# Optimization experiments

Hardware: AMD Instinct MI355X
Metric: run time of the kernel (lower is better)

Reference implementation:

```python
import jax, jax.numpy as jnp
import numpy as np

N = 170000          # n_users + n_entities
NNZ = 2720000       # edges in sparse A_in (avg degree 16)
DIMS = [64, 64, 32, 16]
NEG_SLOPE = 0.01    # nn.LeakyReLU default
EPS = 1e-12         # F.normalize eps


def setup_inputs() -> dict:
    key = jax.random.key(0)
    ks = jax.random.split(key, 20)
    inp = {
        "embeddings": jax.random.normal(ks[0], (N, DIMS[0]), jnp.float32) * 0.1,
        "a_vals": jax.random.uniform(ks[1], (NNZ,), jnp.float32) / 16.0,  # ~row-normalized
    }
    # bi-interaction layer params, stored (in, out) so y = x @ W + b
    i = 2
    for l in range(3):
        din, dout = DIMS[l], DIMS[l + 1]
        s = 1.0 / np.sqrt(din)
        inp[f"w1_{l}"] = jax.random.normal(ks[i], (din, dout), jnp.float32) * s; i += 1
        inp[f"b1_{l}"] = jnp.zeros((dout,), jnp.float32)
        inp[f"w2_{l}"] = jax.random.normal(ks[i], (din, dout), jnp.float32) * s; i += 1
        inp[f"b2_{l}"] = jnp.zeros((dout,), jnp.float32)
    inp["a_rows"] = jax.random.randint(ks[i], (NNZ,), 0, N, jnp.int32); i += 1
    inp["a_cols"] = jax.random.randint(ks[i], (NNZ,), 0, N, jnp.int32)
    return inp


def _leaky(x):
    return jnp.where(x >= 0, x, NEG_SLOPE * x)


def _l2norm(x):
    n = jnp.sqrt(jnp.sum(x * x, axis=1, keepdims=True))
    return x / jnp.maximum(n, EPS)


def _spmm(vals, rows, cols, emb):
    # sparse A (COO) @ emb : gather source rows, scale, scatter-add to dest rows
    msgs = vals[:, None] * emb[cols]          # (nnz, d)
    return jax.ops.segment_sum(msgs, rows, num_segments=N)


def reference(embeddings, a_vals,
              w1_0, b1_0, w2_0, b2_0,
              w1_1, b1_1, w2_1, b2_1,
              w1_2, b1_2, w2_2, b2_2,
              a_rows, a_cols):
    layers = [(w1_0, b1_0, w2_0, b2_0),
              (w1_1, b1_1, w2_1, b2_1),
              (w1_2, b1_2, w2_2, b2_2)]
    ego = embeddings
    all_embed = [ego]
    for (w1, b1, w2, b2) in layers:
        side = _spmm(a_vals, a_rows, a_cols, ego)            # (N, d_in)
        sum_e = _leaky((ego + side) @ w1 + b1)               # bi-interaction
        bi_e = _leaky((ego * side) @ w2 + b2)
        ego = sum_e + bi_e                                   # dropout = identity (eval)
        all_embed.append(_l2norm(ego))
    return jnp.concatenate(all_embed, axis=1)                # (N, 176)
```

## Files before the change

### kernel.cpp

```cpp
#include <hip/hip_runtime.h>
#include <hip/hip_bf16.h>

#define NEG_SLOPE 0.01f
#define L2EPS 1e-12f
#define SCAN_CHUNK 2048
#define PART_CH 8192
#define BSHIFT 9

__device__ __forceinline__ unsigned short f2bf(float f) {
    unsigned u = __float_as_uint(f);
    return (unsigned short)((u + 0x7fffu + ((u >> 16) & 1u)) >> 16);
}


__global__ void scan_sum(const int* __restrict__ counts, int* __restrict__ partials, int n) {
    __shared__ int red[256];
    int base = blockIdx.x * SCAN_CHUNK;
    int s = 0;
    for (int i = threadIdx.x; i < SCAN_CHUNK; i += 256) {
        int idx = base + i;
        s += (idx < n) ? counts[idx] : 0;
    }
    red[threadIdx.x] = s; __syncthreads();
    for (int o = 128; o > 0; o >>= 1) {
        if (threadIdx.x < o) red[threadIdx.x] += red[threadIdx.x + o];
        __syncthreads();
    }
    if (threadIdx.x == 0) partials[blockIdx.x] = red[0];
}

__global__ void scan_partials(int* __restrict__ partials, int nb, int* __restrict__ out, int n) {
    if (threadIdx.x == 0 && blockIdx.x == 0) {
        int run = 0;
        for (int i = 0; i < nb; i++) { int v = partials[i]; partials[i] = run; run += v; }
        out[n] = run;
    }
}

__global__ void scan_apply(const int* __restrict__ counts, const int* __restrict__ partials,
                           int* __restrict__ out, int n) {
    __shared__ int lsum[256];
    int base = blockIdx.x * SCAN_CHUNK;
    int t = threadIdx.x;
    int my[8];
    int s = 0;
    int tb = base + t * 8;
    for (int i = 0; i < 8; i++) { int idx = tb + i; int v = (idx < n) ? counts[idx] : 0; my[i] = v; s += v; }
    lsum[t] = s; __syncthreads();
    for (int o = 1; o < 256; o <<= 1) {
        int v = (t >= o) ? lsum[t - o] : 0;
        __syncthreads();
        lsum[t] += v;
        __syncthreads();
    }
    int excl = lsum[t] - s + partials[blockIdx.x];
    for (int i = 0; i < 8; i++) {
        int idx = tb + i;
        if (idx < n) { out[idx] = excl; excl += my[i]; }
    }
}


__global__ void part_hist(const int* __restrict__ rows, int* __restrict__ hist,
                          int nnz, int nchunks, int B) {
    __shared__ int h[512];
    int c = blockIdx.x;
    for (int i = threadIdx.x; i < B; i += 256) h[i] = 0;
    __syncthreads();
    int s = c * PART_CH, e = min(s + PART_CH, nnz);
    for (int i = s + threadIdx.x; i < e; i += 256) atomicAdd(&h[rows[i] >> BSHIFT], 1);
    __syncthreads();
    for (int b = threadIdx.x; b < B; b += 256) hist[b * nchunks + c] = h[b];
}

__global__ void part_scatter(const int* __restrict__ rows, const int* __restrict__ cols,
                             const float* __restrict__ vals, const int* __restrict__ hscan,
                             int2* __restrict__ tmp, int nnz, int nchunks, int B) {
    __shared__ int cur[512];
    int c = blockIdx.x;
    for (int b = threadIdx.x; b < B; b += 256) cur[b] = hscan[b * nchunks + c];
    __syncthreads();
    int s = c * PART_CH, e = min(s + PART_CH, nnz);
    for (int i = s + threadIdx.x; i < e; i += 256) {
        int r = rows[i];
        int p = atomicAdd(&cur[r >> BSHIFT], 1);
        tmp[p] = make_int2(((r & 511) << 18) | cols[i], __float_as_int(vals[i]));
    }
}

__global__ void bucket_scatter(const int* __restrict__ hscan, const int2* __restrict__ tmp,
                               int2* __restrict__ pedge, int* __restrict__ offsets,
                               int nnz, int nchunks, int B, int n) {
    __shared__ int cnt[512];
    __shared__ int scn[256];
    int b = blockIdx.x;
    int t = threadIdx.x;
    int rbase = b << BSHIFT;
    cnt[t] = 0; cnt[t + 256] = 0;
    __syncthreads();
    int s = hscan[b * nchunks];
    int e = (b == B - 1) ? nnz : hscan[(b + 1) * nchunks];
    for (int j = s + t; j < e; j += 256) atomicAdd(&cnt[((unsigned)tmp[j].x) >> 18], 1);
    __syncthreads();
    int c0 = cnt[2 * t], c1 = cnt[2 * t + 1];
    int ssum = c0 + c1;
    scn[t] = ssum;
    __syncthreads();
    for (int o = 1; o < 256; o <<= 1) {
        int v = (t >= o) ? scn[t - o] : 0;
        __syncthreads();
        scn[t] += v;
        __syncthreads();
    }
    int excl = scn[t] - ssum + s;
    int g0 = rbase + 2 * t, g1 = g0 + 1;
    if (g0 < n) offsets[g0] = excl;
    if (g1 < n) offsets[g1] = excl + c0;
    cnt[2 * t] = excl;
    cnt[2 * t + 1] = excl + c0;
    if (b == B - 1 && t == 0) offsets[n] = nnz;
    __syncthreads();
    for (int j = s + t; j < e; j += 256) {
        int2 tt = tmp[j];
        int r9 = ((unsigned)tt.x) >> 18;
        int p = atomicAdd(&cnt[r9], 1);
        pedge[p] = make_int2(tt.x & 0x3FFFF, tt.y);
    }
}


__global__ void embed_prep(const float* __restrict__ emb, unsigned short* __restrict__ egob,
                           float* __restrict__ outp, int nrows) {
    int idx = blockIdx.x * blockDim.x + threadIdx.x;
    if (idx >= nrows * 16) return;
    int row = idx >> 4, c = idx & 15;
    float4 v = ((const float4*)emb)[idx];
    ((float4*)(outp + (size_t)row * 176))[c] = v;
    ushort4 o;
    o.x = f2bf(v.x); o.y = f2bf(v.y); o.z = f2bf(v.z); o.w = f2bf(v.w);
    ((ushort4*)egob)[idx] = o;
}


__device__ __forceinline__ float leaky1(float x) { return x >= 0.f ? x : NEG_SLOPE * x; }

__device__ __forceinline__ void fma8(float v, uint4 qv, float* acc) {
    acc[0] += v * __uint_as_float(qv.x << 16);
    acc[1] += v * __uint_as_float(qv.x & 0xffff0000u);
    acc[2] += v * __uint_as_float(qv.y << 16);
    acc[3] += v * __uint_as_float(qv.y & 0xffff0000u);
    acc[4] += v * __uint_as_float(qv.z << 16);
    acc[5] += v * __uint_as_float(qv.z & 0xffff0000u);
    acc[6] += v * __uint_as_float(qv.w << 16);
    acc[7] += v * __uint_as_float(qv.w & 0xffff0000u);
}

template <int DIN, int DOUT>
__global__ __launch_bounds__(256, 4)
void fused_layer(const unsigned short* __restrict__ egob, const int* __restrict__ offs,
                 const int2* __restrict__ pedge, const float* __restrict__ ego,
                 const float* __restrict__ w1, const float* __restrict__ b1,
                 const float* __restrict__ w2, const float* __restrict__ b2,
                 float* __restrict__ ego_next, unsigned short* __restrict__ egob_next,
                 float* __restrict__ outp, int col_off, int nrows) {
    constexpr int RPB = 64;
    constexpr int CPL = DIN / 4;
    constexpr int U4  = CPL / 8;
    constexpr int TX  = DOUT / 4;
    constexpr int TY  = 256 / TX;
    constexpr int RPT = RPB / TY;

    __shared__ float sU[DIN][RPB + 4];
    __shared__ float sV[DIN][RPB + 4];

    int tid = threadIdx.x;
    int row0 = blockIdx.x * RPB;

    {
        int r = tid >> 2, q = tid & 3;
        int g = row0 + r;
        float acc[CPL];
#pragma unroll
        for (int i = 0; i < CPL; i++) acc[i] = 0.f;
        if (g < nrows) {
            int j0 = offs[g], j1 = offs[g + 1];
            int j = j0;
            for (; j + 1 < j1; j += 2) {
                int2 e0 = pedge[j];
                int2 e1 = pedge[j + 1];
                float v0 = __int_as_float(e0.y);
                float v1 = __int_as_float(e1.y);
                const uint4* s0 = (const uint4*)(egob + (size_t)e0.x * DIN) + q * U4;
                const uint4* s1 = (const uint4*)(egob + (size_t)e1.x * DIN) + q * U4;
                uint4 qa[U4], qb[U4];
#pragma unroll
                for (int u = 0; u < U4; u++) qa[u] = s0[u];
#pragma unroll
                for (int u = 0; u < U4; u++) qb[u] = s1[u];
#pragma unroll
                for (int u = 0; u < U4; u++) fma8(v0, qa[u], acc + u * 8);
#pragma unroll
                for (int u = 0; u < U4; u++) fma8(v1, qb[u], acc + u * 8);
            }
            if (j < j1) {
                int2 e0 = pedge[j];
                float v0 = __int_as_float(e0.y);
                const uint4* s0 = (const uint4*)(egob + (size_t)e0.x * DIN) + q * U4;
                uint4 qa[U4];
#pragma unroll
                for (int u = 0; u < U4; u++) qa[u] = s0[u];
#pragma unroll
                for (int u = 0; u < U4; u++) fma8(v0, qa[u], acc + u * 8);
            }
            const float4* ep = (const float4*)(ego + (size_t)g * DIN) + q * (CPL / 4);
#pragma unroll
            for (int i = 0; i < CPL / 4; i++) {
                float4 e = ep[i];
                int k0 = q * CPL + i * 4;
                sU[k0 + 0][r] = e.x + acc[i * 4 + 0]; sV[k0 + 0][r] = e.x * acc[i * 4 + 0];
                sU[k0 + 1][r] = e.y + acc[i * 4 + 1]; sV[k0 + 1][r] = e.y * acc[i * 4 + 1];
                sU[k0 + 2][r] = e.z + acc[i * 4 + 2]; sV[k0 + 2][r] = e.z * acc[i * 4 + 2];
                sU[k0 + 3][r] = e.w + acc[i * 4 + 3]; sV[k0 + 3][r] = e.w * acc[i * 4 + 3];
            }
        } else {
#pragma unroll
            for (int i = 0; i < CPL; i++) { sU[q * CPL + i][r] = 0.f; sV[q * CPL + i][r] = 0.f; }
        }
    }
    __syncthreads();

    int tx = tid % TX, ty = tid / TX;
    float4 a1[RPT], a2[RPT];
#pragma unroll
    for (int i = 0; i < RPT; i++) {
        a1[i] = make_float4(0.f, 0.f, 0.f, 0.f);
        a2[i] = make_float4(0.f, 0.f, 0.f, 0.f);
    }

#pragma unroll 8
    for (int k = 0; k < DIN; k++) {
        float4 w1v = ((const float4*)w1)[k * TX + tx];
        float4 w2v = ((const float4*)w2)[k * TX + tx];
        float uv[RPT], vv[RPT];
        if constexpr (RPT == 4) {
            float4 t1 = *(const float4*)&sU[k][ty * 4];
            float4 t2 = *(const float4*)&sV[k][ty * 4];
            uv[0] = t1.x; uv[1] = t1.y; uv[2] = t1.z; uv[3] = t1.w;
            vv[0] = t2.x; vv[1] = t2.y; vv[2] = t2.z; vv[3] = t2.w;
        } else if constexpr (RPT == 2) {
            float2 t1 = *(const float2*)&sU[k][ty * 2];
            float2 t2 = *(const float2*)&sV[k][ty * 2];
            uv[0] = t1.x; uv[1] = t1.y;
            vv[0] = t2.x; vv[1] = t2.y;
        } else {
            uv[0] = sU[k][ty];
            vv[0] = sV[k][ty];
        }
#pragma unroll
        for (int i = 0; i < RPT; i++) {
            a1[i].x += uv[i] * w1v.x; a1[i].y += uv[i] * w1v.y; a1[i].z += uv[i] * w1v.z; a1[i].w += uv[i] * w1v.w;
            a2[i].x += vv[i] * w2v.x; a2[i].y += vv[i] * w2v.y; a2[i].z += vv[i] * w2v.z; a2[i].w += vv[i] * w2v.w;
        }
    }

    float4 bb1 = ((const float4*)b1)[tx];
    float4 bb2 = ((const float4*)b2)[tx];
#pragma unroll
    for (int i = 0; i < RPT; i++) {
        int g = row0 + ty * RPT + i;
        float4 x;
        x.x = leaky1(a1[i].x + bb1.x) + leaky1(a2[i].x + bb2.x);
        x.y = leaky1(a1[i].y + bb1.y) + leaky1(a2[i].y + bb2.y);
        x.z = leaky1(a1[i].z + bb1.z) + leaky1(a2[i].z + bb2.z);
        x.w = leaky1(a1[i].w + bb1.w) + leaky1(a2[i].w + bb2.w);
        float ss = x.x * x.x + x.y * x.y + x.z * x.z + x.w * x.w;
#pragma unroll
        for (int o = TX >> 1; o > 0; o >>= 1) ss += __shfl_xor(ss, o, 64);
        if (g < nrows) {
            if (ego_next) {
                ((float4*)(ego_next + (size_t)g * DOUT))[tx] = x;
                ushort4 xb;
                xb.x = f2bf(x.x); xb.y = f2bf(x.y); xb.z = f2bf(x.z); xb.w = f2bf(x.w);
                ((ushort4*)(egob_next + (size_t)g * DOUT))[tx] = xb;
            }
            float inv = 1.f / fmaxf(sqrtf(ss), L2EPS);
            float4 y = make_float4(x.x * inv, x.y * inv, x.z * inv, x.w * inv);
            ((float4*)(outp + (size_t)g * 176 + col_off))[tx] = y;
        }
    }
}

extern "C" void kernel_launch(void* const* d_in, const int* in_sizes, int n_in,
                              void* d_out, int out_size, void* d_ws, size_t ws_size,
                              hipStream_t stream) {
    const float* emb   = (const float*)d_in[0];
    const float* avals = (const float*)d_in[1];
    const float* w1_0 = (const float*)d_in[2];  const float* b1_0 = (const float*)d_in[3];
    const float* w2_0 = (const float*)d_in[4];  const float* b2_0 = (const float*)d_in[5];
    const float* w1_1 = (const float*)d_in[6];  const float* b1_1 = (const float*)d_in[7];
    const float* w2_1 = (const float*)d_in[8];  const float* b2_1 = (const float*)d_in[9];
    const float* w1_2 = (const float*)d_in[10]; const float* b1_2 = (const float*)d_in[11];
    const float* w2_2 = (const float*)d_in[12]; const float* b2_2 = (const float*)d_in[13];
    const int* arows = (const int*)d_in[14];
    const int* acols = (const int*)d_in[15];
    float* outp = (float*)d_out;

    const int N   = in_sizes[0] / 64;
    const int NNZ = in_sizes[14];

    const int B       = (N + 511) >> BSHIFT;
    const int nchunks = (NNZ + PART_CH - 1) / PART_CH;
    const int NH      = B * nchunks;

    char* w = (char*)d_ws;
    size_t off = 0;
    auto carve = [&](size_t bytes) { char* p = w + off; off += (bytes + 255) & ~(size_t)255; return p; };
    int*   offsets  = (int*)  carve((size_t)(N + 1) * 4);
    int*   partials = (int*)  carve(1024);
    int*   hist     = (int*)  carve((size_t)(NH + 1) * 4);
    int*   hscan    = (int*)  carve((size_t)(NH + 1) * 4);
    int2*  pedge    = (int2*) carve((size_t)NNZ * 8);
    float* ego1     = (float*)carve((size_t)N * 64 * 4);
    float* ego2     = (float*)carve((size_t)N * 32 * 4);
    unsigned short* egobA = (unsigned short*)carve((size_t)N * 64 * 2);
    unsigned short* egobB = (unsigned short*)carve((size_t)N * 64 * 2);
    int2*  tmp      = (int2*)ego1;

    const int NB2 = (NH + SCAN_CHUNK - 1) / SCAN_CHUNK;

    part_hist<<<nchunks, 256, 0, stream>>>(arows, hist, NNZ, nchunks, B);
    scan_sum<<<NB2, 256, 0, stream>>>(hist, partials, NH);
    scan_partials<<<1, 64, 0, stream>>>(partials, NB2, hscan, NH);
    scan_apply<<<NB2, 256, 0, stream>>>(hist, partials, hscan, NH);
    part_scatter<<<nchunks, 256, 0, stream>>>(arows, acols, avals, hscan, tmp, NNZ, nchunks, B);
    bucket_scatter<<<B, 256, 0, stream>>>(hscan, tmp, pedge, offsets, NNZ, nchunks, B, N);

    embed_prep<<<(N * 16 + 255) / 256, 256, 0, stream>>>(emb, egobA, outp, N);

    const int DB = (N + 63) / 64;

    fused_layer<64, 64><<<DB, 256, 0, stream>>>(egobA, offsets, pedge, emb,
                                                w1_0, b1_0, w2_0, b2_0,
                                                ego1, egobB, outp, 64, N);
    fused_layer<64, 32><<<DB, 256, 0, stream>>>(egobB, offsets, pedge, ego1,
                                                w1_1, b1_1, w2_1, b2_1,
                                                ego2, egobA, outp, 128, N);
    fused_layer<32, 16><<<DB, 256, 0, stream>>>(egobA, offsets, pedge, ego2,
                                                w1_2, b1_2, w2_2, b2_2,
                                                nullptr, nullptr, outp, 160, N);
}
```

Measured before the change: 618.6 us.

## Sort rows by degree within block and software-pipeline edge gathers by four

Each block's 64 rows are bitonic-sorted by degree in the first wavefront, so rows of similar degree share a wavefront and divergence in the gather loop drops. The gather loop now issues four edges' loads at once and prefetches the next four edge descriptors, which adds memory-level parallelism. The ego row load is hoisted ahead of the gather. The shared-memory padding is removed, which may bring back bank conflicts in the transposed stores, and the sort adds two syncs plus more register use.

```diff
diff --git a/kernel.cpp b/kernel.cpp
--- a/kernel.cpp
+++ b/kernel.cpp
@@ -170,39 +170,79 @@
     constexpr int TY  = 256 / TX;
     constexpr int RPT = RPB / TY;
 
-    __shared__ float sU[DIN][RPB + 4];
-    __shared__ float sV[DIN][RPB + 4];
+    __shared__ float sU[DIN][RPB];
+    __shared__ float sV[DIN][RPB];
 
     int tid = threadIdx.x;
     int row0 = blockIdx.x * RPB;
 
+    if (tid < 64) {
+        int g = row0 + tid;
+        unsigned deg = (g < nrows) ? (unsigned)(offs[g + 1] - offs[g]) : 0u;
+        unsigned key = (deg << 6) | (unsigned)tid;
+#pragma unroll
+        for (int size = 2; size <= 64; size <<= 1) {
+#pragma unroll
+            for (int stride = size >> 1; stride > 0; stride >>= 1) {
+                unsigned other = __shfl_xor(key, stride, 64);
+                bool dir = ((tid & size) == 0);
+                bool lower = ((tid & stride) == 0);
+                bool takeMin = (lower == dir);
+                key = takeMin ? (key < other ? key : other) : (key > other ? key : other);
+            }
+        }
+        ((int*)sU)[tid] = (int)(key & 63u);
+    }
+    __syncthreads();
+    int r = tid >> 2, q = tid & 3;
+    int pr = ((int*)sU)[r];
+    __syncthreads();
+
     {
-        int r = tid >> 2, q = tid & 3;
-        int g = row0 + r;
+        int g = row0 + pr;
         float acc[CPL];
 #pragma unroll
         for (int i = 0; i < CPL; i++) acc[i] = 0.f;
         if (g < nrows) {
             int j0 = offs[g], j1 = offs[g + 1];
+            float4 erow[CPL / 4];
+            const float4* ep = (const float4*)(ego + (size_t)g * DIN) + q * (CPL / 4);
+#pragma unroll
+            for (int i = 0; i < CPL / 4; i++) erow[i] = ep[i];
+
             int j = j0;
-            for (; j + 1 < j1; j += 2) {
-                int2 e0 = pedge[j];
-                int2 e1 = pedge[j + 1];
-                float v0 = __int_as_float(e0.y);
-                float v1 = __int_as_float(e1.y);
-                const uint4* s0 = (const uint4*)(egob + (size_t)e0.x * DIN) + q * U4;
-                const uint4* s1 = (const uint4*)(egob + (size_t)e1.x * DIN) + q * U4;
-                uint4 qa[U4], qb[U4];
-#pragma unroll
-                for (int u = 0; u < U4; u++) qa[u] = s0[u];
-#pragma unroll
-                for (int u = 0; u < U4; u++) qb[u] = s1[u];
-#pragma unroll
-                for (int u = 0; u < U4; u++) fma8(v0, qa[u], acc + u * 8);
-#pragma unroll
-                for (int u = 0; u < U4; u++) fma8(v1, qb[u], acc + u * 8);
-            }
-            if (j < j1) {
+            int2 ed[4];
+            bool have = (j + 4 <= j1);
+            if (have) {
+#pragma unroll
+                for (int m = 0; m < 4; m++) ed[m] = pedge[j + m];
+            }
+            while (have) {
+                uint4 t[4][U4];
+#pragma unroll
+                for (int m = 0; m < 4; m++) {
+                    const uint4* s = (const uint4*)(egob + (size_t)ed[m].x * DIN) + q * U4;
+#pragma unroll
+                    for (int u = 0; u < U4; u++) t[m][u] = s[u];
+                }
+                bool nxt = (j + 8 <= j1);
+                int2 ed2[4];
+                if (nxt) {
+#pragma unroll
+                    for (int m = 0; m < 4; m++) ed2[m] = pedge[j + 4 + m];
+                }
+#pragma unroll
+                for (int m = 0; m < 4; m++) {
+                    float v = __int_as_float(ed[m].y);
+#pragma unroll
+                    for (int u = 0; u < U4; u++) fma8(v, t[m][u], acc + u * 8);
+                }
+#pragma unroll
+                for (int m = 0; m < 4; m++) ed[m] = ed2[m];
+                j += 4;
+                have = nxt;
+            }
+            for (; j < j1; ++j) {
                 int2 e0 = pedge[j];
                 float v0 = __int_as_float(e0.y);
                 const uint4* s0 = (const uint4*)(egob + (size_t)e0.x * DIN) + q * U4;
@@ -212,19 +252,18 @@
 #pragma unroll
                 for (int u = 0; u < U4; u++) fma8(v0, qa[u], acc + u * 8);
             }
-            const float4* ep = (const float4*)(ego + (size_t)g * DIN) + q * (CPL / 4);
 #pragma unroll
             for (int i = 0; i < CPL / 4; i++) {
-                float4 e = ep[i];
+                float4 e = erow[i];
                 int k0 = q * CPL + i * 4;
-                sU[k0 + 0][r] = e.x + acc[i * 4 + 0]; sV[k0 + 0][r] = e.x * acc[i * 4 + 0];
-                sU[k0 + 1][r] = e.y + acc[i * 4 + 1]; sV[k0 + 1][r] = e.y * acc[i * 4 + 1];
-                sU[k0 + 2][r] = e.z + acc[i * 4 + 2]; sV[k0 + 2][r] = e.z * acc[i * 4 + 2];
-                sU[k0 + 3][r] = e.w + acc[i * 4 + 3]; sV[k0 + 3][r] = e.w * acc[i * 4 + 3];
+                sU[k0 + 0][pr] = e.x + acc[i * 4 + 0]; sV[k0 + 0][pr] = e.x * acc[i * 4 + 0];
+                sU[k0 + 1][pr] = e.y + acc[i * 4 + 1]; sV[k0 + 1][pr] = e.y * acc[i * 4 + 1];
+                sU[k0 + 2][pr] = e.z + acc[i * 4 + 2]; sV[k0 + 2][pr] = e.z * acc[i * 4 + 2];
+                sU[k0 + 3][pr] = e.w + acc[i * 4 + 3]; sV[k0 + 3][pr] = e.w * acc[i * 4 + 3];
             }
         } else {
 #pragma unroll
-            for (int i = 0; i < CPL; i++) { sU[q * CPL + i][r] = 0.f; sV[q * CPL + i][r] = 0.f; }
+            for (int i = 0; i < CPL; i++) { sU[q * CPL + i][pr] = 0.f; sV[q * CPL + i][pr] = 0.f; }
         }
     }
     __syncthreads();
```

Measured after the change: 613.7 us. No clear change (-0.8%).
